# Performance work log

Hardware: AMD Instinct MI355X
Metric: run time of the kernel (lower is better)

## Reference

```python
import jax, jax.numpy as jnp
import numpy as np

N, C_IN, C_OUT, HID, H = 4096, 512, 512, 128, 4
HEAD_OUT = C_OUT // H  # 128
MID = 4 * C_OUT        # 2048
R = 1.0                # spatial radius r
L = 48                 # sequence window l
NEG = -1e9


def layer_norm(x, g, b, eps=1e-5):
    m = jnp.mean(x, axis=-1, keepdims=True)
    v = jnp.mean(jnp.square(x - m), axis=-1, keepdims=True)
    return (x - m) * jax.lax.rsqrt(v + eps) * g + b


def setup_inputs() -> dict:
    key = jax.random.key(0)
    ks = jax.random.split(key, 16)
    s = lambda fan: 1.0 / np.sqrt(fan)
    return {
        "x":   jax.random.normal(ks[0], (N, C_IN), jnp.float32),
        "pos": jax.random.normal(ks[1], (N, 3), jnp.float32),
        "ori": jax.random.normal(ks[2], (N, 3), jnp.float32),
        "seq": jnp.arange(N, dtype=jnp.int64) if jax.config.jax_enable_x64 else jnp.arange(N, dtype=jnp.int32),
        "batch": jnp.sort(jax.random.randint(ks[3], (N,), 0, 8)),
        "ln1_g": jnp.ones((C_IN,), jnp.float32),
        "ln1_b": jnp.zeros((C_IN,), jnp.float32),
        "ln2_g": jnp.ones((C_OUT,), jnp.float32),
        "ln2_b": jnp.zeros((C_OUT,), jnp.float32),
        "Wq": jax.random.normal(ks[4], (H, C_IN, HID), jnp.float32) * s(C_IN),
        "Wk": jax.random.normal(ks[5], (H, C_IN, HID), jnp.float32) * s(C_IN),
        "Wv": jax.random.normal(ks[6], (H, C_IN, HID), jnp.float32) * s(C_IN),
        "Wo": jax.random.normal(ks[7], (H, HID, HEAD_OUT), jnp.float32) * s(HID),
        "lnm_g": jnp.ones((MID,), jnp.float32),
        "lnm_b": jnp.zeros((MID,), jnp.float32),
        "W1": jax.random.normal(ks[8], (C_OUT, MID), jnp.float32) * s(C_OUT),
        "W2": jax.random.normal(ks[9], (MID, C_OUT), jnp.float32) * s(MID),
    }


def _block(x, pos, ori, seq, batch, ln1_g, ln1_b, ln2_g, ln2_b,
           Wq, Wk, Wv, Wo, lnm_g, lnm_b, W1, W2):
    identity = x
    xn = layer_norm(x, ln1_g, ln1_b)

    # geometry/sequence neighborhood mask: same graph, ||dp||<=r, |ds|<=l
    d2 = jnp.sum(jnp.square(pos[:, None, :] - pos[None, :, :]), axis=-1)  # [N,N]
    ds = jnp.abs(seq[:, None] - seq[None, :])
    mask = (batch[:, None] == batch[None, :]) & (d2 <= R * R) & (ds <= L)

    # all heads at once (original loops over heads; math identical)
    q = jnp.einsum('nc,hcd->hnd', xn, Wq)
    k = jnp.einsum('nc,hcd->hnd', xn, Wk)
    v = jnp.einsum('nc,hcd->hnd', xn, Wv)
    gbias = ori @ ori.T  # geometric orientation bias [N,N]
    scores = jnp.einsum('hnd,hmd->hnm', q, k) / np.sqrt(HID) + gbias[None]
    scores = jnp.where(mask[None], scores, NEG)
    attn = jax.nn.softmax(scores, axis=-1)
    o = jnp.einsum('hnm,hmd->hnd', attn, v)
    o = jnp.einsum('hnd,hde->hne', o, Wo)               # [H,N,HEAD_OUT]
    o = jnp.transpose(o, (1, 0, 2)).reshape(N, C_OUT)   # concat heads

    x = o + identity
    identity = x
    h = layer_norm(x, ln2_g, ln2_b) @ W1
    h = jax.nn.relu(layer_norm(h, lnm_g, lnm_b))
    return h @ W2 + identity


def reference(x, pos, ori, seq, batch, ln1_g, ln1_b, ln2_g, ln2_b,
              Wq, Wk, Wv, Wo, lnm_g, lnm_b, W1, W2):
    return _block(x, pos, ori, seq, batch, ln1_g, ln1_b, ln2_g, ln2_b,
                  Wq, Wk, Wv, Wo, lnm_g, lnm_b, W1, W2)
```

## Files before the change

kernel.cpp:

```cpp
#include <hip/hip_runtime.h>

typedef unsigned short u16;
typedef unsigned int u32;
typedef float f32x4 __attribute__((ext_vector_type(4)));
typedef __bf16 bf16x8 __attribute__((ext_vector_type(8)));

#define N_TOK 4096
#define QKV_LD 1536
#define NH 4
#define HID 128
#define C_OUT 512

__device__ __forceinline__ float b2f(u16 u) { return __uint_as_float(((u32)u) << 16); }
__device__ __forceinline__ u16 f2b(float f) {
  u32 u = __float_as_uint(f);
  u32 r = (u + 0x7fffu + ((u >> 16) & 1u)) >> 16;
  return (u16)r;
}

__global__ __launch_bounds__(256) void transpose_tile(
    const float* __restrict__ src, u16* __restrict__ dst, int R, int C)
{
  __shared__ u16 tile[32][33];
  const int b = blockIdx.z;
  const int c0 = blockIdx.x * 32, r0 = blockIdx.y * 32;
  const int tx = threadIdx.x & 31, ty = threadIdx.x >> 5;
  const float* s = src + (size_t)b * R * C;
  u16* d = dst + (size_t)b * R * C;
#pragma unroll
  for (int i = 0; i < 32; i += 8)
    tile[ty + i][tx] = f2b(s[(size_t)(r0 + ty + i) * C + c0 + tx]);
  __syncthreads();
#pragma unroll
  for (int i = 0; i < 32; i += 8)
    d[(size_t)(c0 + ty + i) * R + r0 + tx] = tile[tx][ty + i];
}

__global__ __launch_bounds__(256) void transpose_all(
    const float* __restrict__ Wq, const float* __restrict__ Wk,
    const float* __restrict__ Wv, const float* __restrict__ Wo,
    const float* __restrict__ W1,
    u16* __restrict__ Btqkv, u16* __restrict__ Wot, u16* __restrict__ W1t)
{
  __shared__ u16 tile[32][33];
  const int idx = blockIdx.x;
  const float* s; u16* d; int R, C, r0, c0;
  if (idx < 1024) {
    s = W1; d = W1t; R = 512; C = 2048;
    r0 = (idx >> 6) * 32; c0 = (idx & 63) * 32;
  } else if (idx < 1792) {
    int i = idx - 1024;
    int z = i >> 6, rem = i & 63;
    int which = z >> 2, b = z & 3;
    const float* base = (which == 0) ? Wq : (which == 1) ? Wk : Wv;
    s = base + (size_t)b * 512 * 128;
    d = Btqkv + (size_t)which * 4 * 512 * 128 + (size_t)b * 512 * 128;
    R = 512; C = 128;
    r0 = (rem >> 2) * 32; c0 = (rem & 3) * 32;
  } else {
    int i = idx - 1792;
    int b = i >> 4, rem = i & 15;
    s = Wo + (size_t)b * 128 * 128;
    d = Wot + (size_t)b * 128 * 128;
    R = 128; C = 128;
    r0 = (rem >> 2) * 32; c0 = (rem & 3) * 32;
  }
  const int tx = threadIdx.x & 31, ty = threadIdx.x >> 5;
#pragma unroll
  for (int i = 0; i < 32; i += 8)
    tile[ty + i][tx] = f2b(s[(size_t)(r0 + ty + i) * C + c0 + tx]);
  __syncthreads();
#pragma unroll
  for (int i = 0; i < 32; i += 8)
    d[(size_t)(c0 + ty + i) * R + r0 + tx] = tile[tx][ty + i];
}

__global__ __launch_bounds__(256) void ln512_f32(
    const float* __restrict__ x, const float* __restrict__ g,
    const float* __restrict__ b, u16* __restrict__ y)
{
  const int lane = threadIdx.x & 63;
  const int row = blockIdx.x * 4 + (threadIdx.x >> 6);
  const float* xr = x + (size_t)row * 512;
  const int c = lane * 8;
  float4 a0 = *(const float4*)(xr + c);
  float4 a1 = *(const float4*)(xr + c + 4);
  float v[8] = {a0.x, a0.y, a0.z, a0.w, a1.x, a1.y, a1.z, a1.w};
  float s1 = 0.f, s2 = 0.f;
#pragma unroll
  for (int i = 0; i < 8; i++) { s1 += v[i]; s2 += v[i] * v[i]; }
#pragma unroll
  for (int o = 32; o; o >>= 1) { s1 += __shfl_xor(s1, o); s2 += __shfl_xor(s2, o); }
  float mean = s1 * (1.f / 512.f);
  float var = s2 * (1.f / 512.f) - mean * mean;
  float rs = rsqrtf(fmaxf(var, 0.f) + 1e-5f);
  float4 g0 = *(const float4*)(g + c), g1 = *(const float4*)(g + c + 4);
  float4 b0 = *(const float4*)(b + c), b1 = *(const float4*)(b + c + 4);
  float gg[8] = {g0.x, g0.y, g0.z, g0.w, g1.x, g1.y, g1.z, g1.w};
  float bb[8] = {b0.x, b0.y, b0.z, b0.w, b1.x, b1.y, b1.z, b1.w};
  u16 t[8];
#pragma unroll
  for (int i = 0; i < 8; i++) t[i] = f2b((v[i] - mean) * rs * gg[i] + bb[i]);
  *(uint4*)(y + (size_t)row * 512 + c) = *(const uint4*)t;
}

__global__ __launch_bounds__(256) void ln2048_bf16_relu(
    const u16* __restrict__ x, const float* __restrict__ g,
    const float* __restrict__ b, u16* __restrict__ y)
{
  const int row = blockIdx.x, tid = threadIdx.x;
  const int c = tid * 8;
  const u16* xr = x + (size_t)row * 2048;
  uint4 u = *(const uint4*)(xr + c);
  u16 e[8]; *(uint4*)e = u;
  float v[8];
#pragma unroll
  for (int i = 0; i < 8; i++) v[i] = b2f(e[i]);
  float s1 = 0.f, s2 = 0.f;
#pragma unroll
  for (int i = 0; i < 8; i++) { s1 += v[i]; s2 += v[i] * v[i]; }
#pragma unroll
  for (int o = 32; o; o >>= 1) { s1 += __shfl_xor(s1, o); s2 += __shfl_xor(s2, o); }
  __shared__ float red[2][4];
  int lane = tid & 63, w = tid >> 6;
  if (lane == 0) { red[0][w] = s1; red[1][w] = s2; }
  __syncthreads();
  s1 = red[0][0] + red[0][1] + red[0][2] + red[0][3];
  s2 = red[1][0] + red[1][1] + red[1][2] + red[1][3];
  float mean = s1 * (1.f / 2048.f);
  float var = s2 * (1.f / 2048.f) - mean * mean;
  float rs = rsqrtf(fmaxf(var, 0.f) + 1e-5f);
  float4 g0 = *(const float4*)(g + c), g1 = *(const float4*)(g + c + 4);
  float4 b0 = *(const float4*)(b + c), b1 = *(const float4*)(b + c + 4);
  float gg[8] = {g0.x, g0.y, g0.z, g0.w, g1.x, g1.y, g1.z, g1.w};
  float bb[8] = {b0.x, b0.y, b0.z, b0.w, b1.x, b1.y, b1.z, b1.w};
  u16 t[8];
#pragma unroll
  for (int i = 0; i < 8; i++)
    t[i] = f2b(fmaxf((v[i] - mean) * rs * gg[i] + bb[i], 0.f));
  *(uint4*)(y + (size_t)row * 2048 + c) = *(const uint4*)t;
}

#define LDK 40
__global__ __launch_bounds__(512, 4) void gemm128(
    const u16* __restrict__ A, int lda,
    const u16* __restrict__ Bt,
    void* __restrict__ C, int ldc, int outf32,
    const float* __restrict__ res,
    int Kslice, int Ktot, int bd, int atomic)
{
  __shared__ u16 As[128 * LDK];
  __shared__ u16 Bs[128 * LDK];
  const int bn = blockIdx.x, bm = blockIdx.y;
  const int m0 = bm * 128, n0 = bn * 128;
  const int kbase = blockIdx.z * Kslice;
  const int abase = (bd ? bn * Ktot : 0) + kbase;
  const int tid = threadIdx.x;
  const int lane = tid & 63, w = tid >> 6;
  const int wm = (w & 1) * 64;
  const int wn = (w >> 1) * 32;
  const int l16 = lane & 15, quad = lane >> 4;

  const int sr = tid >> 2, sc = (tid & 3) * 8;
  const u16* PA = A + (size_t)(m0 + sr) * lda + abase + sc;
  const u16* PB = Bt + (size_t)(n0 + sr) * Ktot + kbase + sc;

  f32x4 acc[4][2];
#pragma unroll
  for (int i = 0; i < 4; i++)
#pragma unroll
    for (int j = 0; j < 2; j++) acc[i][j] = (f32x4){0.f, 0.f, 0.f, 0.f};

  int4 pa = *(const int4*)PA;
  int4 pb = *(const int4*)PB;
  for (int kk = 0; kk < Kslice; kk += 32) {
    *(int4*)&As[sr * LDK + sc] = pa;
    *(int4*)&Bs[sr * LDK + sc] = pb;
    __syncthreads();
    if (kk + 32 < Kslice) {
      PA += 32; pa = *(const int4*)PA;
      PB += 32; pb = *(const int4*)PB;
    }
    bf16x8 af[4], bfr[2];
#pragma unroll
    for (int mt = 0; mt < 4; mt++)
      af[mt] = *(const bf16x8*)&As[(wm + mt * 16 + l16) * LDK + quad * 8];
#pragma unroll
    for (int nt = 0; nt < 2; nt++)
      bfr[nt] = *(const bf16x8*)&Bs[(wn + nt * 16 + l16) * LDK + quad * 8];
#pragma unroll
    for (int mt = 0; mt < 4; mt++)
#pragma unroll
      for (int nt = 0; nt < 2; nt++)
        acc[mt][nt] = __builtin_amdgcn_mfma_f32_16x16x32_bf16(
            af[mt], bfr[nt], acc[mt][nt], 0, 0, 0);
    __syncthreads();
  }

#pragma unroll
  for (int mt = 0; mt < 4; mt++)
#pragma unroll
    for (int nt = 0; nt < 2; nt++)
#pragma unroll
      for (int r = 0; r < 4; r++) {
        int gr = m0 + wm + mt * 16 + quad * 4 + r;
        int gc = n0 + wn + nt * 16 + l16;
        size_t off = (size_t)gr * ldc + gc;
        float v = acc[mt][nt][r];
        if (atomic) {
          atomicAdd((float*)C + off, v);
        } else {
          if (res) v += res[off];
          if (outf32) ((float*)C)[off] = v;
          else        ((u16*)C)[off] = f2b(v);
        }
      }
}

#define TQ 16
#define BAND 112
#define KROW 136
#define PROW 120
__global__ __launch_bounds__(256) void attn_mfma(
    const u16* __restrict__ qkv, const float* __restrict__ pos,
    const float* __restrict__ ori, const int* __restrict__ batch,
    const u16* __restrict__ wot, const float* __restrict__ xres,
    float* __restrict__ out)
{
  const int h = blockIdx.y;
  const int bxs = (blockIdx.x & 7) * 32 + (blockIdx.x >> 3);
  const int i0 = bxs * TQ;
  const int j0 = i0 - 48;
  const int tid = threadIdx.x;
  const int lane = tid & 63, w = tid >> 6;
  const int l16 = lane & 15, quad = lane >> 4;

  __shared__ u16 kv[128 * KROW];
  __shared__ u16 qp[TQ * KROW];
  __shared__ float ps[TQ * PROW];
  __shared__ float bpx[BAND], bpy[BAND], bpz[BAND];
  __shared__ float box_[BAND], boy_[BAND], boz_[BAND];
  __shared__ int bb[BAND];

  for (int t = tid; t < BAND; t += 256) {
    int j = j0 + t;
    if (j >= 0 && j < N_TOK) {
      bpx[t] = pos[j * 3 + 0]; bpy[t] = pos[j * 3 + 1]; bpz[t] = pos[j * 3 + 2];
      box_[t] = ori[j * 3 + 0]; boy_[t] = ori[j * 3 + 1]; boz_[t] = ori[j * 3 + 2];
      bb[t] = batch[j];
    } else {
      bpx[t] = bpy[t] = bpz[t] = 0.f;
      box_[t] = boy_[t] = boz_[t] = 0.f;
      bb[t] = -12345;
    }
  }
  for (int idx = tid; idx < BAND * 16; idx += 256) {
    int t = idx >> 4, c8 = (idx & 15) * 8;
    int j = j0 + t;
    int4 val = {0, 0, 0, 0};
    if (j >= 0 && j < N_TOK)
      val = *(const int4*)&qkv[(size_t)j * QKV_LD + 512 + h * HID + c8];
    *(int4*)&kv[t * KROW + c8] = val;
  }
  {
    int q = tid >> 4, c8 = (tid & 15) * 8;
    *(int4*)&qp[q * KROW + c8] =
        *(const int4*)&qkv[(size_t)(i0 + q) * QKV_LD + h * HID + c8];
  }
  __syncthreads();

  {
    bf16x8 af[4];
#pragma unroll
    for (int kc = 0; kc < 4; kc++)
      af[kc] = *(const bf16x8*)&qp[l16 * KROW + kc * 32 + quad * 8];
#pragma unroll
    for (int ti = 0; ti < 2; ti++) {
      int tt = w + ti * 4;
      if (tt < 7) {
        f32x4 acc = (f32x4){0.f, 0.f, 0.f, 0.f};
#pragma unroll
        for (int kc = 0; kc < 4; kc++) {
          bf16x8 bf = *(const bf16x8*)&kv[(tt * 16 + l16) * KROW + kc * 32 + quad * 8];
          acc = __builtin_amdgcn_mfma_f32_16x16x32_bf16(af[kc], bf, acc, 0, 0, 0);
        }
        int t = tt * 16 + l16;
#pragma unroll
        for (int r = 0; r < 4; r++) {
          int q = quad * 4 + r, iq = q + 48;
          int dseq = iq - t;
          bool ok = (bb[t] == bb[iq]) && (dseq <= 48) && (dseq >= -48);
          {
#pragma clang fp contract(off)
            float dx = bpx[iq] - bpx[t], dy = bpy[iq] - bpy[t], dz = bpz[iq] - bpz[t];
            float d2 = dx * dx + dy * dy + dz * dz;
            ok = ok && (d2 <= 1.0f);
          }
          float s = -1e9f;
          if (ok) {
            float gb = box_[iq] * box_[t] + boy_[iq] * boy_[t] + boz_[iq] * boz_[t];
            s = acc[r] * 0.08838834764831845f + gb;
          }
          ps[q * PROW + t] = s;
        }
      }
    }
  }
  __syncthreads();

  for (int idx = tid; idx < BAND * 32; idx += 256) {
    int t = idx >> 5, d4 = (idx & 31) * 4;
    int j = j0 + t;
    uint2 val; val.x = 0; val.y = 0;
    if (j >= 0 && j < N_TOK)
      val = *(const uint2*)&qkv[(size_t)j * QKV_LD + 1024 + h * HID + d4];
    u16 e[4] = {(u16)val.x, (u16)(val.x >> 16), (u16)val.y, (u16)(val.y >> 16)};
#pragma unroll
    for (int jj = 0; jj < 4; jj++) {
      int dd = (jj + tid) & 3;
      kv[(d4 + dd) * KROW + t] = e[dd];
    }
  }
  for (int idx = tid; idx < 128 * 16; idx += 256) {
    int d = idx >> 4, t = BAND + (idx & 15);
    kv[d * KROW + t] = 0;
  }
  {
    int row = tid >> 4, sub = tid & 15;
    float vals[7];
    float m = -1e30f;
#pragma unroll
    for (int i = 0; i < 7; i++) {
      vals[i] = ps[row * PROW + sub + i * 16];
      m = fmaxf(m, vals[i]);
    }
#pragma unroll
    for (int o = 8; o; o >>= 1) m = fmaxf(m, __shfl_xor(m, o));
    float s = 0.f;
#pragma unroll
    for (int i = 0; i < 7; i++) { vals[i] = __expf(vals[i] - m); s += vals[i]; }
#pragma unroll
    for (int o = 8; o; o >>= 1) s += __shfl_xor(s, o);
    float inv = 1.f / s;
#pragma unroll
    for (int i = 0; i < 7; i++)
      qp[row * KROW + sub + i * 16] = f2b(vals[i] * inv);
    qp[row * KROW + BAND + sub] = 0;
  }
  __syncthreads();

  u16 obuf[2][4];
  {
    bf16x8 paf[4];
#pragma unroll
    for (int kc = 0; kc < 4; kc++)
      paf[kc] = *(const bf16x8*)&qp[l16 * KROW + kc * 32 + quad * 8];
#pragma unroll
    for (int ti = 0; ti < 2; ti++) {
      int dt = w + ti * 4;
      f32x4 acc = (f32x4){0.f, 0.f, 0.f, 0.f};
#pragma unroll
      for (int kc = 0; kc < 4; kc++) {
        bf16x8 bf = *(const bf16x8*)&kv[(dt * 16 + l16) * KROW + kc * 32 + quad * 8];
        acc = __builtin_amdgcn_mfma_f32_16x16x32_bf16(paf[kc], bf, acc, 0, 0, 0);
      }
#pragma unroll
      for (int r = 0; r < 4; r++) obuf[ti][r] = f2b(acc[r]);
    }
  }
  __syncthreads();

#pragma unroll
  for (int ti = 0; ti < 2; ti++) {
    int dt = w + ti * 4;
#pragma unroll
    for (int r = 0; r < 4; r++)
      qp[(quad * 4 + r) * KROW + dt * 16 + l16] = obuf[ti][r];
  }
  {
    const u16* wsrc = wot + (size_t)h * HID * HID;
    for (int idx = tid; idx < 128 * 16; idx += 256) {
      int e = idx >> 4, c8 = (idx & 15) * 8;
      *(int4*)&kv[e * KROW + c8] = *(const int4*)&wsrc[e * HID + c8];
    }
  }
  __syncthreads();

  {
    bf16x8 oaf[4];
#pragma unroll
    for (int kc = 0; kc < 4; kc++)
      oaf[kc] = *(const bf16x8*)&qp[l16 * KROW + kc * 32 + quad * 8];
#pragma unroll
    for (int ti = 0; ti < 2; ti++) {
      int et = w + ti * 4;
      f32x4 acc = (f32x4){0.f, 0.f, 0.f, 0.f};
#pragma unroll
      for (int kc = 0; kc < 4; kc++) {
        bf16x8 bf = *(const bf16x8*)&kv[(et * 16 + l16) * KROW + kc * 32 + quad * 8];
        acc = __builtin_amdgcn_mfma_f32_16x16x32_bf16(oaf[kc], bf, acc, 0, 0, 0);
      }
#pragma unroll
      for (int r = 0; r < 4; r++) {
        int q = quad * 4 + r;
        size_t off = (size_t)(i0 + q) * C_OUT + h * HID + et * 16 + l16;
        out[off] = acc[r] + xres[off];
      }
    }
  }
}

#define MB (1048576)
extern "C" void kernel_launch(void* const* d_in, const int* in_sizes, int n_in,
                              void* d_out, int out_size, void* d_ws, size_t ws_size,
                              hipStream_t stream) {
  const float* x    = (const float*)d_in[0];
  const float* pos  = (const float*)d_in[1];
  const float* ori  = (const float*)d_in[2];
  const int*   batch = (const int*)d_in[4];
  const float* ln1g = (const float*)d_in[5];
  const float* ln1b = (const float*)d_in[6];
  const float* ln2g = (const float*)d_in[7];
  const float* ln2b = (const float*)d_in[8];
  const float* Wq = (const float*)d_in[9];
  const float* Wk = (const float*)d_in[10];
  const float* Wv = (const float*)d_in[11];
  const float* Wo = (const float*)d_in[12];
  const float* lnmg = (const float*)d_in[13];
  const float* lnmb = (const float*)d_in[14];
  const float* W1 = (const float*)d_in[15];
  const float* W2 = (const float*)d_in[16];
  float* out = (float*)d_out;

  char* ws = (char*)d_ws;
  u16* xn    = (u16*)(ws + 0);
  u16* x1n   = (u16*)(ws + 0);
  u16* qkv   = (u16*)(ws + 4 * MB);
  u16* h     = (u16*)(ws + 4 * MB);
  u16* Wot   = (u16*)(ws + 16 * MB);
  u16* Btqkv = (u16*)(ws + 20 * MB);
  u16* W2t   = (u16*)(ws + 20 * MB);
  u16* W1t   = (u16*)(ws + 22 * MB);

  transpose_all<<<dim3(1856), 256, 0, stream>>>(Wq, Wk, Wv, Wo, W1,
                                                Btqkv, Wot, W1t);
  ln512_f32<<<dim3(1024), 256, 0, stream>>>(x, ln1g, ln1b, xn);
  gemm128<<<dim3(12, 32, 1), 512, 0, stream>>>(xn, 512, Btqkv, qkv, QKV_LD, 0,
                                               nullptr, 512, 512, 0, 0);
  transpose_tile<<<dim3(16, 64, 1), 256, 0, stream>>>(W2, W2t, 2048, 512);
  attn_mfma<<<dim3(256, NH), 256, 0, stream>>>(qkv, pos, ori, batch, Wot, x, out);
  ln512_f32<<<dim3(1024), 256, 0, stream>>>(out, ln2g, ln2b, x1n);
  gemm128<<<dim3(16, 32, 1), 512, 0, stream>>>(x1n, 512, W1t, h, 2048, 0,
                                               nullptr, 512, 512, 0, 0);
  ln2048_bf16_relu<<<dim3(4096), 256, 0, stream>>>(h, lnmg, lnmb, h);
  gemm128<<<dim3(4, 32, 2), 512, 0, stream>>>(h, 2048, W2t, out, 512, 1,
                                              nullptr, 1024, 2048, 0, 1);
}
```

Measured before the change: 200.5 us.

## Fuse prep kernels, hide W2 transpose in attention, double-buffer GEMM via direct LDS loads

```diff
diff --git a/kernel.cpp b/kernel.cpp
--- a/kernel.cpp
+++ b/kernel.cpp
@@ -18,15 +18,16 @@
   return (u16)r;
 }
 
-__global__ __launch_bounds__(256) void transpose_tile(
-    const float* __restrict__ src, u16* __restrict__ dst, int R, int C)
-{
-  __shared__ u16 tile[32][33];
-  const int b = blockIdx.z;
-  const int c0 = blockIdx.x * 32, r0 = blockIdx.y * 32;
+__device__ __forceinline__ void gload16(const u16* g, u16* l) {
+  __builtin_amdgcn_global_load_lds(
+      (const __attribute__((address_space(1))) void*)g,
+      (__attribute__((address_space(3))) void*)l, 16, 0, 0);
+}
+
+__device__ __forceinline__ void tr32(const float* __restrict__ s,
+                                     u16* __restrict__ d, int R, int C,
+                                     int r0, int c0, u16 (*tile)[33]) {
   const int tx = threadIdx.x & 31, ty = threadIdx.x >> 5;
-  const float* s = src + (size_t)b * R * C;
-  u16* d = dst + (size_t)b * R * C;
 #pragma unroll
   for (int i = 0; i < 32; i += 8)
     tile[ty + i][tx] = f2b(s[(size_t)(r0 + ty + i) * C + c0 + tx]);
@@ -36,14 +37,48 @@
     d[(size_t)(c0 + ty + i) * R + r0 + tx] = tile[tx][ty + i];
 }
 
-__global__ __launch_bounds__(256) void transpose_all(
+__device__ __forceinline__ void ln512_body(
+    const float* __restrict__ x, const float* __restrict__ g,
+    const float* __restrict__ b, u16* __restrict__ y, int row) {
+  const int lane = threadIdx.x & 63;
+  const float* xr = x + (size_t)row * 512;
+  const int c = lane * 8;
+  float4 a0 = *(const float4*)(xr + c);
+  float4 a1 = *(const float4*)(xr + c + 4);
+  float v[8] = {a0.x, a0.y, a0.z, a0.w, a1.x, a1.y, a1.z, a1.w};
+  float s1 = 0.f, s2 = 0.f;
+#pragma unroll
+  for (int i = 0; i < 8; i++) { s1 += v[i]; s2 += v[i] * v[i]; }
+#pragma unroll
+  for (int o = 32; o; o >>= 1) { s1 += __shfl_xor(s1, o); s2 += __shfl_xor(s2, o); }
+  float mean = s1 * (1.f / 512.f);
+  float var = s2 * (1.f / 512.f) - mean * mean;
+  float rs = rsqrtf(fmaxf(var, 0.f) + 1e-5f);
+  float4 g0 = *(const float4*)(g + c), g1 = *(const float4*)(g + c + 4);
+  float4 b0 = *(const float4*)(b + c), b1 = *(const float4*)(b + c + 4);
+  float gg[8] = {g0.x, g0.y, g0.z, g0.w, g1.x, g1.y, g1.z, g1.w};
+  float bb[8] = {b0.x, b0.y, b0.z, b0.w, b1.x, b1.y, b1.z, b1.w};
+  u16 t[8];
+#pragma unroll
+  for (int i = 0; i < 8; i++) t[i] = f2b((v[i] - mean) * rs * gg[i] + bb[i]);
+  *(uint4*)(y + (size_t)row * 512 + c) = *(const uint4*)t;
+}
+
+__global__ __launch_bounds__(256) void prep(
+    const float* __restrict__ x, const float* __restrict__ ln1g,
+    const float* __restrict__ ln1b, u16* __restrict__ xn,
     const float* __restrict__ Wq, const float* __restrict__ Wk,
     const float* __restrict__ Wv, const float* __restrict__ Wo,
     const float* __restrict__ W1,
     u16* __restrict__ Btqkv, u16* __restrict__ Wot, u16* __restrict__ W1t)
 {
   __shared__ u16 tile[32][33];
-  const int idx = blockIdx.x;
+  const int bid = blockIdx.x;
+  if (bid < 1024) {
+    ln512_body(x, ln1g, ln1b, xn, bid * 4 + (threadIdx.x >> 6));
+    return;
+  }
+  const int idx = bid - 1024;
   const float* s; u16* d; int R, C, r0, c0;
   if (idx < 1024) {
     s = W1; d = W1t; R = 512; C = 2048;
@@ -65,43 +100,14 @@
     R = 128; C = 128;
     r0 = (rem >> 2) * 32; c0 = (rem & 3) * 32;
   }
-  const int tx = threadIdx.x & 31, ty = threadIdx.x >> 5;
-#pragma unroll
-  for (int i = 0; i < 32; i += 8)
-    tile[ty + i][tx] = f2b(s[(size_t)(r0 + ty + i) * C + c0 + tx]);
-  __syncthreads();
-#pragma unroll
-  for (int i = 0; i < 32; i += 8)
-    d[(size_t)(c0 + ty + i) * R + r0 + tx] = tile[tx][ty + i];
+  tr32(s, d, R, C, r0, c0, tile);
 }
 
 __global__ __launch_bounds__(256) void ln512_f32(
     const float* __restrict__ x, const float* __restrict__ g,
     const float* __restrict__ b, u16* __restrict__ y)
 {
-  const int lane = threadIdx.x & 63;
-  const int row = blockIdx.x * 4 + (threadIdx.x >> 6);
-  const float* xr = x + (size_t)row * 512;
-  const int c = lane * 8;
-  float4 a0 = *(const float4*)(xr + c);
-  float4 a1 = *(const float4*)(xr + c + 4);
-  float v[8] = {a0.x, a0.y, a0.z, a0.w, a1.x, a1.y, a1.z, a1.w};
-  float s1 = 0.f, s2 = 0.f;
-#pragma unroll
-  for (int i = 0; i < 8; i++) { s1 += v[i]; s2 += v[i] * v[i]; }
-#pragma unroll
-  for (int o = 32; o; o >>= 1) { s1 += __shfl_xor(s1, o); s2 += __shfl_xor(s2, o); }
-  float mean = s1 * (1.f / 512.f);
-  float var = s2 * (1.f / 512.f) - mean * mean;
-  float rs = rsqrtf(fmaxf(var, 0.f) + 1e-5f);
-  float4 g0 = *(const float4*)(g + c), g1 = *(const float4*)(g + c + 4);
-  float4 b0 = *(const float4*)(b + c), b1 = *(const float4*)(b + c + 4);
-  float gg[8] = {g0.x, g0.y, g0.z, g0.w, g1.x, g1.y, g1.z, g1.w};
-  float bb[8] = {b0.x, b0.y, b0.z, b0.w, b1.x, b1.y, b1.z, b1.w};
-  u16 t[8];
-#pragma unroll
-  for (int i = 0; i < 8; i++) t[i] = f2b((v[i] - mean) * rs * gg[i] + bb[i]);
-  *(uint4*)(y + (size_t)row * 512 + c) = *(const uint4*)t;
+  ln512_body(x, g, b, y, blockIdx.x * 4 + (threadIdx.x >> 6));
 }
 
 __global__ __launch_bounds__(256) void ln2048_bf16_relu(
@@ -141,29 +147,31 @@
   *(uint4*)(y + (size_t)row * 2048 + c) = *(const uint4*)t;
 }
 
-#define LDK 40
 __global__ __launch_bounds__(512, 4) void gemm128(
     const u16* __restrict__ A, int lda,
     const u16* __restrict__ Bt,
     void* __restrict__ C, int ldc, int outf32,
     const float* __restrict__ res,
-    int Kslice, int Ktot, int bd, int atomic)
+    int Kslice, int Ktot, int atomic)
 {
-  __shared__ u16 As[128 * LDK];
-  __shared__ u16 Bs[128 * LDK];
+  __shared__ u16 As[2][128 * 32];
+  __shared__ u16 Bs[2][128 * 32];
   const int bn = blockIdx.x, bm = blockIdx.y;
   const int m0 = bm * 128, n0 = bn * 128;
   const int kbase = blockIdx.z * Kslice;
-  const int abase = (bd ? bn * Ktot : 0) + kbase;
   const int tid = threadIdx.x;
   const int lane = tid & 63, w = tid >> 6;
   const int wm = (w & 1) * 64;
   const int wn = (w >> 1) * 32;
   const int l16 = lane & 15, quad = lane >> 4;
 
-  const int sr = tid >> 2, sc = (tid & 3) * 8;
-  const u16* PA = A + (size_t)(m0 + sr) * lda + abase + sc;
-  const u16* PB = Bt + (size_t)(n0 + sr) * Ktot + kbase + sc;
+  const int r_st = tid >> 2;
+  const int chunk = (tid & 3) ^ ((tid >> 3) & 3);
+  const u16* PA = A + (size_t)(m0 + r_st) * lda + kbase + chunk * 8;
+  const u16* PB = Bt + (size_t)(n0 + r_st) * Ktot + kbase + chunk * 8;
+  const int wbase = w * 512;
+
+  const int slot8 = (quad ^ ((l16 >> 1) & 3)) * 8;
 
   f32x4 acc[4][2];
 #pragma unroll
@@ -171,23 +179,24 @@
 #pragma unroll
     for (int j = 0; j < 2; j++) acc[i][j] = (f32x4){0.f, 0.f, 0.f, 0.f};
 
-  int4 pa = *(const int4*)PA;
-  int4 pb = *(const int4*)PB;
+  gload16(PA, &As[0][wbase]);
+  gload16(PB, &Bs[0][wbase]);
+  __syncthreads();
+
+  int buf = 0;
   for (int kk = 0; kk < Kslice; kk += 32) {
-    *(int4*)&As[sr * LDK + sc] = pa;
-    *(int4*)&Bs[sr * LDK + sc] = pb;
-    __syncthreads();
     if (kk + 32 < Kslice) {
-      PA += 32; pa = *(const int4*)PA;
-      PB += 32; pb = *(const int4*)PB;
+      PA += 32; PB += 32;
+      gload16(PA, &As[buf ^ 1][wbase]);
+      gload16(PB, &Bs[buf ^ 1][wbase]);
     }
     bf16x8 af[4], bfr[2];
 #pragma unroll
     for (int mt = 0; mt < 4; mt++)
-      af[mt] = *(const bf16x8*)&As[(wm + mt * 16 + l16) * LDK + quad * 8];
+      af[mt] = *(const bf16x8*)&As[buf][(wm + mt * 16 + l16) * 32 + slot8];
 #pragma unroll
     for (int nt = 0; nt < 2; nt++)
-      bfr[nt] = *(const bf16x8*)&Bs[(wn + nt * 16 + l16) * LDK + quad * 8];
+      bfr[nt] = *(const bf16x8*)&Bs[buf][(wn + nt * 16 + l16) * 32 + slot8];
 #pragma unroll
     for (int mt = 0; mt < 4; mt++)
 #pragma unroll
@@ -195,6 +204,7 @@
         acc[mt][nt] = __builtin_amdgcn_mfma_f32_16x16x32_bf16(
             af[mt], bfr[nt], acc[mt][nt], 0, 0, 0);
     __syncthreads();
+    buf ^= 1;
   }
 
 #pragma unroll
@@ -225,8 +235,23 @@
     const u16* __restrict__ qkv, const float* __restrict__ pos,
     const float* __restrict__ ori, const int* __restrict__ batch,
     const u16* __restrict__ wot, const float* __restrict__ xres,
-    float* __restrict__ out)
+    float* __restrict__ out,
+    const float* __restrict__ W2, u16* __restrict__ W2t)
 {
+  __shared__ u16 kv[128 * KROW];
+  __shared__ u16 qp[TQ * KROW];
+  __shared__ float ps[TQ * PROW];
+  __shared__ float bpx[BAND], bpy[BAND], bpz[BAND];
+  __shared__ float box_[BAND], boy_[BAND], boz_[BAND];
+  __shared__ int bb[BAND];
+
+  if (blockIdx.x >= 256) {
+    int idx = (blockIdx.x - 256) + blockIdx.y * 256;
+    int r0 = (idx >> 4) * 32, c0 = (idx & 15) * 32;
+    tr32(W2, W2t, 2048, 512, r0, c0, (u16(*)[33])kv);
+    return;
+  }
+
   const int h = blockIdx.y;
   const int bxs = (blockIdx.x & 7) * 32 + (blockIdx.x >> 3);
   const int i0 = bxs * TQ;
@@ -234,13 +259,6 @@
   const int tid = threadIdx.x;
   const int lane = tid & 63, w = tid >> 6;
   const int l16 = lane & 15, quad = lane >> 4;
-
-  __shared__ u16 kv[128 * KROW];
-  __shared__ u16 qp[TQ * KROW];
-  __shared__ float ps[TQ * PROW];
-  __shared__ float bpx[BAND], bpy[BAND], bpz[BAND];
-  __shared__ float box_[BAND], boy_[BAND], boz_[BAND];
-  __shared__ int bb[BAND];
 
   for (int t = tid; t < BAND; t += 256) {
     int j = j0 + t;
@@ -442,17 +460,16 @@
   u16* W2t   = (u16*)(ws + 20 * MB);
   u16* W1t   = (u16*)(ws + 22 * MB);
 
-  transpose_all<<<dim3(1856), 256, 0, stream>>>(Wq, Wk, Wv, Wo, W1,
-                                                Btqkv, Wot, W1t);
-  ln512_f32<<<dim3(1024), 256, 0, stream>>>(x, ln1g, ln1b, xn);
+  prep<<<dim3(2880), 256, 0, stream>>>(x, ln1g, ln1b, xn,
+                                       Wq, Wk, Wv, Wo, W1, Btqkv, Wot, W1t);
   gemm128<<<dim3(12, 32, 1), 512, 0, stream>>>(xn, 512, Btqkv, qkv, QKV_LD, 0,
-                                               nullptr, 512, 512, 0, 0);
-  transpose_tile<<<dim3(16, 64, 1), 256, 0, stream>>>(W2, W2t, 2048, 512);
-  attn_mfma<<<dim3(256, NH), 256, 0, stream>>>(qkv, pos, ori, batch, Wot, x, out);
+                                               nullptr, 512, 512, 0);
+  attn_mfma<<<dim3(512, NH), 256, 0, stream>>>(qkv, pos, ori, batch, Wot, x, out,
+                                               W2, W2t);
   ln512_f32<<<dim3(1024), 256, 0, stream>>>(out, ln2g, ln2b, x1n);
   gemm128<<<dim3(16, 32, 1), 512, 0, stream>>>(x1n, 512, W1t, h, 2048, 0,
-                                               nullptr, 512, 512, 0, 0);
+                                               nullptr, 512, 512, 0);
   ln2048_bf16_relu<<<dim3(4096), 256, 0, stream>>>(h, lnmg, lnmb, h);
   gemm128<<<dim3(4, 32, 2), 512, 0, stream>>>(h, 2048, W2t, out, 512, 1,
-                                              nullptr, 1024, 2048, 0, 1);
-}
+                                              nullptr, 1024, 2048, 1);
+}
```

Result: faster. 193.9 us (-3.3%).
